# Performance work log

Measured on AMD Instinct MI355X. Metric: run time of the kernel, lower is better.

The kernel has to match this reference:

```python
import jax, jax.numpy as jnp
import numpy as np

HOPS = 3
VOCAB, EMBD, STORY_LEN, SENT_LEN, BATCH, QLEN = 50000, 128, 200, 32, 64, 32
INIT_RNG = 0.1


def setup_inputs() -> dict:
    key = jax.random.key(0)
    k1, k2, k3, k4, k5 = jax.random.split(key, 5)
    x = jax.random.randint(k1, (BATCH, STORY_LEN, SENT_LEN), 0, VOCAB)          # story token ids
    q = jax.random.randint(k2, (BATCH, QLEN), 0, VOCAB)                          # question token ids
    # hops+1 embedding tables, initialized ~ Normal(mean=-0.1, std=0.1) as in the torch code
    A = jax.random.normal(k3, (HOPS + 1, VOCAB, EMBD), dtype=jnp.float32) * INIT_RNG - INIT_RNG
    TA = jax.random.normal(k4, (STORY_LEN,), dtype=jnp.float32) * INIT_RNG - INIT_RNG
    TC = jax.random.normal(k5, (STORY_LEN,), dtype=jnp.float32) * INIT_RNG - INIT_RNG
    return {"A": A, "TA": TA, "TC": TC, "x": x, "q": q}


def reference(A, TA, TC, x, q):
    # dropout p=0.0 -> identity
    # u: question embedding, summed over query tokens -> [B, E]
    u = jnp.take(A[1], q, axis=0).sum(axis=1)
    for k in range(HOPS):
        # memory (m) and output (c) representations: gather + sum over sentence tokens + temporal encoding
        m = jnp.take(A[k], x, axis=0).sum(axis=2) + TA[None, :, None]      # [B, S, E]
        c = jnp.take(A[k + 1], x, axis=0).sum(axis=2) + TC[None, :, None]  # [B, S, E]
        p = jax.nn.softmax(jnp.einsum("bse,be->bs", m, u), axis=-1)        # attention over story [B, S]
        u = jnp.einsum("bse,bs->be", c, p) + u                              # weighted combine + residual
    logits = u @ A[HOPS].T                                                  # W = A[-1].weight.T -> [B, V]
    return jax.nn.log_softmax(logits, axis=-1)
```

## Files before the change

kernel.cpp:

```cpp
#include <hip/hip_runtime.h>
#include <math.h>

#define VOCAB 50000
#define EMBD  128
#define SLEN  200
#define TOK   32
#define BATCH 64
#define QLEN  32
#define NSENT (BATCH*SLEN)
#define NTASK (4*NSENT + BATCH)
#define TBL   ((size_t)VOCAB*EMBD)
#define VT    32
#define NTILE ((VOCAB + VT - 1)/VT)

__device__ inline float bits2f(unsigned u){ union{unsigned u; float f;}c; c.u=u; return c.f; }
__device__ inline unsigned f2bits(float f){ union{float f; unsigned u;}c; c.f=f; return c.u; }
__device__ inline unsigned pack_bf16(float lo, float hi){
    unsigned ul = f2bits(lo), uh = f2bits(hi);
    unsigned rl = (ul + 0x7fffu + ((ul>>16)&1u)) >> 16;
    unsigned rh = (uh + 0x7fffu + ((uh>>16)&1u)) >> 16;
    return rl | (rh<<16);
}

__device__ inline float waveSum(float v) {
    #pragma unroll
    for (int o = 32; o > 0; o >>= 1) v += __shfl_down(v, o, 64);
    return v;
}
__device__ inline float waveMax(float v) {
    #pragma unroll
    for (int o = 32; o > 0; o >>= 1) v = fmaxf(v, __shfl_down(v, o, 64));
    return v;
}

__global__ __launch_bounds__(256) void conv_kernel(
    const float* __restrict__ A, unsigned* __restrict__ Ab)
{
    size_t i = ((size_t)blockIdx.x*256 + threadIdx.x)*8;
    float4 a = *(const float4*)(A+i);
    float4 b = *(const float4*)(A+i+4);
    uint4 o;
    o.x = pack_bf16(a.x,a.y); o.y = pack_bf16(a.z,a.w);
    o.z = pack_bf16(b.x,b.y); o.w = pack_bf16(b.z,b.w);
    *(uint4*)(Ab + i/2) = o;
}

__global__ __launch_bounds__(256) void gather_kernel(
    const unsigned* __restrict__ Ab, const int* __restrict__ x,
    const int* __restrict__ q, float* __restrict__ G, float* __restrict__ uF)
{
    int w    = blockIdx.x * 4 + (threadIdx.x >> 6);
    int lane = threadIdx.x & 63;
    const int*      idxp;
    const unsigned* tbl;
    float*          outp;
    if (w < 4 * NSENT) {
        int k  = w / NSENT;
        int bs = w - k * NSENT;
        idxp = x + (size_t)bs * TOK;
        tbl  = Ab + (size_t)k * (TBL/2);
        outp = G + (size_t)w * EMBD;
    } else {
        int b = w - 4 * NSENT;
        idxp = q + (size_t)b * QLEN;
        tbl  = Ab + (TBL/2);
        outp = uF + (size_t)b * EMBD;
    }
    int tg = lane >> 4;
    int sl = lane & 15;
    int idxs[8];
    #pragma unroll
    for (int i = 0; i < 8; i++) idxs[i] = idxp[i*4 + tg];
    float acc[8];
    #pragma unroll
    for (int c = 0; c < 8; c++) acc[c] = 0.f;
    #pragma unroll
    for (int i = 0; i < 8; i++) {
        uint4 v = *(const uint4*)(tbl + (size_t)idxs[i]*64 + sl*4);
        acc[0] += bits2f(v.x<<16); acc[1] += bits2f(v.x&0xffff0000u);
        acc[2] += bits2f(v.y<<16); acc[3] += bits2f(v.y&0xffff0000u);
        acc[4] += bits2f(v.z<<16); acc[5] += bits2f(v.z&0xffff0000u);
        acc[6] += bits2f(v.w<<16); acc[7] += bits2f(v.w&0xffff0000u);
    }
    #pragma unroll
    for (int c = 0; c < 8; c++) {
        acc[c] += __shfl_xor(acc[c], 32, 64);
        acc[c] += __shfl_xor(acc[c], 16, 64);
    }
    if (lane < 32) {
        int g = lane & 15, h = lane >> 4;
        float4 r; r.x = acc[4*h]; r.y = acc[4*h+1]; r.z = acc[4*h+2]; r.w = acc[4*h+3];
        ((float4*)outp)[2*g + h] = r;
    }
}

__global__ __launch_bounds__(1024) void hops_kernel(
    const float* __restrict__ G, float* __restrict__ u,
    const float* __restrict__ TA, const float* __restrict__ TC)
{
    int b = blockIdx.x;
    int t = threadIdx.x;
    int lane = t & 63, wid = t >> 6;
    __shared__ __align__(16) float uL[EMBD];
    __shared__ float p[256];
    __shared__ float red[16], red2[16];
    __shared__ float pc[7*EMBD];

    if (t < EMBD) uL[t] = u[(size_t)b * EMBD + t];
    __syncthreads();

    for (int k = 0; k < 3; k++) {
        float v = (t < EMBD) ? uL[t] : 0.f;
        v = waveSum(v);
        if (lane == 0) red[wid] = v;
        __syncthreads();
        float sumU = 0.f;
        #pragma unroll
        for (int i = 0; i < 16; i++) sumU += red[i];
        int s = t >> 2, qd = t & 3;
        if (s < SLEN) {
            const float4* g4 = (const float4*)(G + ((size_t)k*NSENT + (size_t)b*SLEN + s)*EMBD);
            const float4* u4 = (const float4*)uL;
            float dot = 0.f;
            #pragma unroll
            for (int e = 0; e < 8; e++) {
                float4 gg = g4[qd*8+e], uu = u4[qd*8+e];
                dot += gg.x*uu.x + gg.y*uu.y + gg.z*uu.z + gg.w*uu.w;
            }
            dot += __shfl_xor(dot, 1, 64);
            dot += __shfl_xor(dot, 2, 64);
            if (qd == 0) p[s] = dot + TA[s]*sumU;
        }
        __syncthreads();
        float mv = (t < SLEN) ? p[t] : -3.4e38f;
        mv = waveMax(mv);
        if (lane == 0) red[wid] = mv;
        __syncthreads();
        float M = -3.4e38f;
        #pragma unroll
        for (int i = 0; i < 16; i++) M = fmaxf(M, red[i]);
        __syncthreads();
        float ev = 0.f, tc = 0.f;
        if (t < SLEN) { ev = __expf(p[t] - M); p[t] = ev; tc = ev * TC[t]; }
        float sv = waveSum(ev);
        float tv = waveSum(tc);
        if (lane == 0) { red[wid] = sv; red2[wid] = tv; }
        __syncthreads();
        float sumP = 0.f, pTC = 0.f;
        #pragma unroll
        for (int i = 0; i < 16; i++) { sumP += red[i]; pTC += red2[i]; }
        const float* Gc = G + ((size_t)(k+1)*NSENT + (size_t)b*SLEN)*EMBD;
        int e = t & 127, ch = t >> 7;
        float acc = 0.f;
        for (int s2 = ch*25; s2 < ch*25 + 25; s2++)
            acc += p[s2] * Gc[(size_t)s2*EMBD + e];
        if (ch > 0) pc[(ch-1)*EMBD + e] = acc;
        __syncthreads();
        if (ch == 0) {
            #pragma unroll
            for (int c = 0; c < 7; c++) acc += pc[c*EMBD + e];
            uL[e] += (acc + pTC) / sumP;
        }
        __syncthreads();
    }
    if (t < EMBD) u[(size_t)b * EMBD + t] = uL[t];
}

__global__ __launch_bounds__(256) void logits_kernel(
    const unsigned* __restrict__ A3b, const float* __restrict__ u,
    float* __restrict__ out, float* __restrict__ part)
{
    __shared__ __align__(16) float Us[BATCH * EMBD];
    __shared__ __align__(16) float As[VT * 132];
    int t  = threadIdx.x;
    int v0 = blockIdx.x * VT;
    #pragma unroll
    for (int pp = 0; pp < 8; pp++) {
        int f = t * 4 + pp * 1024;
        *(float4*)&Us[f] = *(const float4*)&u[f];
    }
    {
        int f = t * 16;
        int r = f >> 7, c = f & 127;
        int vv = v0 + r;
        float vals[16];
        if (vv < VOCAB) {
            const unsigned* src = A3b + (size_t)vv*64 + (c>>1);
            uint4 p0 = *(const uint4*)src;
            uint4 p1 = *(const uint4*)(src + 4);
            vals[0]=bits2f(p0.x<<16);  vals[1]=bits2f(p0.x&0xffff0000u);
            vals[2]=bits2f(p0.y<<16);  vals[3]=bits2f(p0.y&0xffff0000u);
            vals[4]=bits2f(p0.z<<16);  vals[5]=bits2f(p0.z&0xffff0000u);
            vals[6]=bits2f(p0.w<<16);  vals[7]=bits2f(p0.w&0xffff0000u);
            vals[8]=bits2f(p1.x<<16);  vals[9]=bits2f(p1.x&0xffff0000u);
            vals[10]=bits2f(p1.y<<16); vals[11]=bits2f(p1.y&0xffff0000u);
            vals[12]=bits2f(p1.z<<16); vals[13]=bits2f(p1.z&0xffff0000u);
            vals[14]=bits2f(p1.w<<16); vals[15]=bits2f(p1.w&0xffff0000u);
        } else {
            #pragma unroll
            for (int i = 0; i < 16; i++) vals[i] = 0.f;
        }
        #pragma unroll
        for (int i = 0; i < 16; i += 4)
            *(float4*)&As[r*132 + c + i] = *(float4*)&vals[i];
    }
    __syncthreads();
    int lane = t & 63, w = t >> 6;
    int tx = lane & 15, ty = lane >> 4;
    int bb = w * 16 + ty * 4;
    float acc[4][2];
    #pragma unroll
    for (int i = 0; i < 4; i++) { acc[i][0] = 0.f; acc[i][1] = 0.f; }
    for (int k = 0; k < EMBD; k += 4) {
        float4 a[2], uu[4];
        a[0] = *(float4*)&As[tx * 132 + k];
        a[1] = *(float4*)&As[(tx + 16) * 132 + k];
        #pragma unroll
        for (int i = 0; i < 4; i++) uu[i] = *(float4*)&Us[(bb + i) * EMBD + k];
        #pragma unroll
        for (int i = 0; i < 4; i++)
            #pragma unroll
            for (int j = 0; j < 2; j++)
                acc[i][j] += uu[i].x * a[j].x + uu[i].y * a[j].y
                           + uu[i].z * a[j].z + uu[i].w * a[j].w;
    }
    bool val0 = (v0 + tx) < VOCAB, val1 = (v0 + tx + 16) < VOCAB;
    #pragma unroll
    for (int i = 0; i < 4; i++) {
        int bI = bb + i;
        if (val0) out[(size_t)bI * VOCAB + v0 + tx]      = acc[i][0];
        if (val1) out[(size_t)bI * VOCAB + v0 + tx + 16] = acc[i][1];
        float m = fmaxf(val0 ? acc[i][0] : -3.4e38f, val1 ? acc[i][1] : -3.4e38f);
        #pragma unroll
        for (int o = 1; o < 16; o <<= 1) m = fmaxf(m, __shfl_xor(m, o, 64));
        float se = (val0 ? __expf(acc[i][0] - m) : 0.f)
                 + (val1 ? __expf(acc[i][1] - m) : 0.f);
        #pragma unroll
        for (int o = 1; o < 16; o <<= 1) se += __shfl_xor(se, o, 64);
        if (tx == 0) {
            float2 pr; pr.x = m; pr.y = se;
            ((float2*)part)[(size_t)bI * NTILE + blockIdx.x] = pr;
        }
    }
}

__global__ __launch_bounds__(256) void lse_kernel(
    const float* __restrict__ part, float* __restrict__ lse)
{
    int r = blockIdx.x, t = threadIdx.x;
    int lane = t & 63, wid = t >> 6;
    __shared__ float sm[4], sl[4];
    const float2* P = (const float2*)part + (size_t)r * NTILE;
    float M = -3.4e38f, L = 0.f;
    for (int i = t; i < NTILE; i += 256) {
        float2 pr = P[i];
        float m2 = fmaxf(M, pr.x);
        L = L * __expf(M - m2) + pr.y * __expf(pr.x - m2);
        M = m2;
    }
    #pragma unroll
    for (int o = 1; o < 64; o <<= 1) {
        float Mo = __shfl_xor(M, o, 64), Lo = __shfl_xor(L, o, 64);
        float m2 = fmaxf(M, Mo);
        L = L * __expf(M - m2) + Lo * __expf(Mo - m2);
        M = m2;
    }
    if (lane == 0) { sm[wid] = M; sl[wid] = L; }
    __syncthreads();
    if (t == 0) {
        float Mf = -3.4e38f, Lf = 0.f;
        #pragma unroll
        for (int i = 0; i < 4; i++) {
            float m2 = fmaxf(Mf, sm[i]);
            Lf = Lf * __expf(Mf - m2) + sl[i] * __expf(sm[i] - m2);
            Mf = m2;
        }
        lse[r] = Mf + __logf(Lf);
    }
}

__global__ __launch_bounds__(256) void norm_kernel(
    float* __restrict__ out, const float* __restrict__ lse)
{
    int gid = blockIdx.x * 256 + threadIdx.x;
    int b = gid / (VOCAB/4);
    float l = lse[b];
    float4 v = ((float4*)out)[gid];
    v.x -= l; v.y -= l; v.z -= l; v.w -= l;
    ((float4*)out)[gid] = v;
}

extern "C" void kernel_launch(void* const* d_in, const int* in_sizes, int n_in,
                              void* d_out, int out_size, void* d_ws, size_t ws_size,
                              hipStream_t stream)
{
    const float* A  = (const float*)d_in[0];
    const float* TA = (const float*)d_in[1];
    const float* TC = (const float*)d_in[2];
    const int*   x  = (const int*)d_in[3];
    const int*   q  = (const int*)d_in[4];
    float* out = (float*)d_out;

    unsigned* Ab = (unsigned*)d_ws;
    float* G   = (float*)((char*)d_ws + (size_t)4*TBL*2);
    float* uF  = G + (size_t)4*NSENT*EMBD;
    float* part= uF + (size_t)BATCH*EMBD;
    float* lse = part + (size_t)BATCH*NTILE*2;

    conv_kernel  <<<12500, 256, 0, stream>>>(A, Ab);
    gather_kernel<<<NTASK/4, 256, 0, stream>>>(Ab, x, q, G, uF);
    hops_kernel  <<<BATCH, 1024, 0, stream>>>(G, uF, TA, TC);
    logits_kernel<<<NTILE, 256, 0, stream>>>(Ab + 3*(TBL/2), uF, out, part);
    lse_kernel   <<<BATCH, 256, 0, stream>>>(part, lse);
    norm_kernel  <<<BATCH*(VOCAB/4)/256, 256, 0, stream>>>(out, lse);
}
```

Before: 283.4 us.

## Use bf16 MFMA for logits, cache G in LDS across hops, fuse lse into norm

```diff
diff --git a/kernel.cpp b/kernel.cpp
--- a/kernel.cpp
+++ b/kernel.cpp
@@ -10,8 +10,10 @@
 #define NSENT (BATCH*SLEN)
 #define NTASK (4*NSENT + BATCH)
 #define TBL   ((size_t)VOCAB*EMBD)
-#define VT    32
-#define NTILE ((VOCAB + VT - 1)/VT)
+#define NTILE 3125
+
+typedef short short8 __attribute__((ext_vector_type(8)));
+typedef float f32x4  __attribute__((ext_vector_type(4)));
 
 __device__ inline float bits2f(unsigned u){ union{unsigned u; float f;}c; c.u=u; return c.f; }
 __device__ inline unsigned f2bits(float f){ union{float f; unsigned u;}c; c.f=f; return c.u; }
@@ -21,6 +23,10 @@
     unsigned rh = (uh + 0x7fffu + ((uh>>16)&1u)) >> 16;
     return rl | (rh<<16);
 }
+__device__ inline unsigned short bf16of(float f){
+    unsigned u = f2bits(f);
+    return (unsigned short)((u + 0x7fffu + ((u>>16)&1u)) >> 16);
+}
 
 __device__ inline float waveSum(float v) {
     #pragma unroll
@@ -49,12 +55,22 @@
     const unsigned* __restrict__ Ab, const int* __restrict__ x,
     const int* __restrict__ q, float* __restrict__ G, float* __restrict__ uF)
 {
-    int w    = blockIdx.x * 4 + (threadIdx.x >> 6);
+    int B = blockIdx.x;
+    int wid = threadIdx.x >> 6;
+    int w;
+    if (B < 12800) {
+        int k = (B & 7) >> 1;
+        int i = (B >> 3)*2 + (B & 1);
+        w = k*NSENT + i*4 + wid;
+    } else {
+        w = B*4 + wid;
+    }
     int lane = threadIdx.x & 63;
     const int*      idxp;
     const unsigned* tbl;
-    float*          outp;
-    if (w < 4 * NSENT) {
+    bool qtask = (w >= 4*NSENT);
+    float* outp;
+    if (!qtask) {
         int k  = w / NSENT;
         int bs = w - k * NSENT;
         idxp = x + (size_t)bs * TOK;
@@ -95,18 +111,20 @@
 }
 
 __global__ __launch_bounds__(1024) void hops_kernel(
-    const float* __restrict__ G, float* __restrict__ u,
-    const float* __restrict__ TA, const float* __restrict__ TC)
+    const float* __restrict__ G, const float* __restrict__ uF,
+    const float* __restrict__ TA, const float* __restrict__ TC,
+    unsigned short* __restrict__ ub)
 {
     int b = blockIdx.x;
     int t = threadIdx.x;
     int lane = t & 63, wid = t >> 6;
+    __shared__ __align__(16) float Gs[SLEN*132];
     __shared__ __align__(16) float uL[EMBD];
     __shared__ float p[256];
     __shared__ float red[16], red2[16];
     __shared__ float pc[7*EMBD];
 
-    if (t < EMBD) uL[t] = u[(size_t)b * EMBD + t];
+    if (t < EMBD) uL[t] = uF[(size_t)b * EMBD + t];
     __syncthreads();
 
     for (int k = 0; k < 3; k++) {
@@ -119,13 +137,22 @@
         for (int i = 0; i < 16; i++) sumU += red[i];
         int s = t >> 2, qd = t & 3;
         if (s < SLEN) {
-            const float4* g4 = (const float4*)(G + ((size_t)k*NSENT + (size_t)b*SLEN + s)*EMBD);
             const float4* u4 = (const float4*)uL;
             float dot = 0.f;
-            #pragma unroll
-            for (int e = 0; e < 8; e++) {
-                float4 gg = g4[qd*8+e], uu = u4[qd*8+e];
-                dot += gg.x*uu.x + gg.y*uu.y + gg.z*uu.z + gg.w*uu.w;
+            if (k == 0) {
+                const float4* g4 = (const float4*)(G + ((size_t)b*SLEN + s)*EMBD);
+                #pragma unroll
+                for (int e = 0; e < 8; e++) {
+                    float4 gg = g4[qd*8+e], uu = u4[qd*8+e];
+                    dot += gg.x*uu.x + gg.y*uu.y + gg.z*uu.z + gg.w*uu.w;
+                }
+            } else {
+                const float4* g4 = (const float4*)(Gs + s*132);
+                #pragma unroll
+                for (int e = 0; e < 8; e++) {
+                    float4 gg = g4[qd*8+e], uu = u4[qd*8+e];
+                    dot += gg.x*uu.x + gg.y*uu.y + gg.z*uu.z + gg.w*uu.w;
+                }
             }
             dot += __shfl_xor(dot, 1, 64);
             dot += __shfl_xor(dot, 2, 64);
@@ -152,8 +179,11 @@
         const float* Gc = G + ((size_t)(k+1)*NSENT + (size_t)b*SLEN)*EMBD;
         int e = t & 127, ch = t >> 7;
         float acc = 0.f;
-        for (int s2 = ch*25; s2 < ch*25 + 25; s2++)
-            acc += p[s2] * Gc[(size_t)s2*EMBD + e];
+        for (int s2 = ch*25; s2 < ch*25 + 25; s2++) {
+            float g = Gc[(size_t)s2*EMBD + e];
+            Gs[s2*132 + e] = g;
+            acc += p[s2] * g;
+        }
         if (ch > 0) pc[(ch-1)*EMBD + e] = acc;
         __syncthreads();
         if (ch == 0) {
@@ -163,94 +193,69 @@
         }
         __syncthreads();
     }
-    if (t < EMBD) u[(size_t)b * EMBD + t] = uL[t];
-}
-
-__global__ __launch_bounds__(256) void logits_kernel(
-    const unsigned* __restrict__ A3b, const float* __restrict__ u,
+    if (t < EMBD) ub[(size_t)b * EMBD + t] = bf16of(uL[t]);
+}
+
+__global__ __launch_bounds__(256) void logits_mfma(
+    const unsigned short* __restrict__ A3b, const unsigned short* __restrict__ ub,
     float* __restrict__ out, float* __restrict__ part)
 {
-    __shared__ __align__(16) float Us[BATCH * EMBD];
-    __shared__ __align__(16) float As[VT * 132];
-    int t  = threadIdx.x;
-    int v0 = blockIdx.x * VT;
-    #pragma unroll
-    for (int pp = 0; pp < 8; pp++) {
-        int f = t * 4 + pp * 1024;
-        *(float4*)&Us[f] = *(const float4*)&u[f];
-    }
-    {
-        int f = t * 16;
-        int r = f >> 7, c = f & 127;
-        int vv = v0 + r;
-        float vals[16];
-        if (vv < VOCAB) {
-            const unsigned* src = A3b + (size_t)vv*64 + (c>>1);
-            uint4 p0 = *(const uint4*)src;
-            uint4 p1 = *(const uint4*)(src + 4);
-            vals[0]=bits2f(p0.x<<16);  vals[1]=bits2f(p0.x&0xffff0000u);
-            vals[2]=bits2f(p0.y<<16);  vals[3]=bits2f(p0.y&0xffff0000u);
-            vals[4]=bits2f(p0.z<<16);  vals[5]=bits2f(p0.z&0xffff0000u);
-            vals[6]=bits2f(p0.w<<16);  vals[7]=bits2f(p0.w&0xffff0000u);
-            vals[8]=bits2f(p1.x<<16);  vals[9]=bits2f(p1.x&0xffff0000u);
-            vals[10]=bits2f(p1.y<<16); vals[11]=bits2f(p1.y&0xffff0000u);
-            vals[12]=bits2f(p1.z<<16); vals[13]=bits2f(p1.z&0xffff0000u);
-            vals[14]=bits2f(p1.w<<16); vals[15]=bits2f(p1.w&0xffff0000u);
-        } else {
+    int w = blockIdx.x*4 + (threadIdx.x >> 6);
+    if (w >= NTILE) return;
+    int lane = threadIdx.x & 63;
+    int col = lane & 15, quad = lane >> 4;
+    int v0 = w * 16;
+
+    short8 af[4][4];
+    #pragma unroll
+    for (int bt = 0; bt < 4; bt++)
+        #pragma unroll
+        for (int kc = 0; kc < 4; kc++)
+            af[bt][kc] = *(const short8*)(ub + (bt*16 + col)*EMBD + kc*32 + quad*8);
+
+    f32x4 acc[4];
+    #pragma unroll
+    for (int bt = 0; bt < 4; bt++) acc[bt] = (f32x4){0.f, 0.f, 0.f, 0.f};
+
+    #pragma unroll
+    for (int kc = 0; kc < 4; kc++) {
+        short8 bf = *(const short8*)(A3b + (size_t)(v0 + col)*EMBD + kc*32 + quad*8);
+        #pragma unroll
+        for (int bt = 0; bt < 4; bt++)
+            acc[bt] = __builtin_amdgcn_mfma_f32_16x16x32_bf16(af[bt][kc], bf, acc[bt], 0, 0, 0);
+    }
+
+    #pragma unroll
+    for (int bt = 0; bt < 4; bt++) {
+        #pragma unroll
+        for (int r = 0; r < 4; r++) {
+            int bI = bt*16 + quad*4 + r;
+            out[(size_t)bI * VOCAB + v0 + col] = acc[bt][r];
+        }
+        #pragma unroll
+        for (int r = 0; r < 4; r++) {
+            float m = acc[bt][r];
             #pragma unroll
-            for (int i = 0; i < 16; i++) vals[i] = 0.f;
-        }
-        #pragma unroll
-        for (int i = 0; i < 16; i += 4)
-            *(float4*)&As[r*132 + c + i] = *(float4*)&vals[i];
-    }
-    __syncthreads();
-    int lane = t & 63, w = t >> 6;
-    int tx = lane & 15, ty = lane >> 4;
-    int bb = w * 16 + ty * 4;
-    float acc[4][2];
-    #pragma unroll
-    for (int i = 0; i < 4; i++) { acc[i][0] = 0.f; acc[i][1] = 0.f; }
-    for (int k = 0; k < EMBD; k += 4) {
-        float4 a[2], uu[4];
-        a[0] = *(float4*)&As[tx * 132 + k];
-        a[1] = *(float4*)&As[(tx + 16) * 132 + k];
-        #pragma unroll
-        for (int i = 0; i < 4; i++) uu[i] = *(float4*)&Us[(bb + i) * EMBD + k];
-        #pragma unroll
-        for (int i = 0; i < 4; i++)
+            for (int o = 1; o < 16; o <<= 1) m = fmaxf(m, __shfl_xor(m, o, 64));
+            float se = __expf(acc[bt][r] - m);
             #pragma unroll
-            for (int j = 0; j < 2; j++)
-                acc[i][j] += uu[i].x * a[j].x + uu[i].y * a[j].y
-                           + uu[i].z * a[j].z + uu[i].w * a[j].w;
-    }
-    bool val0 = (v0 + tx) < VOCAB, val1 = (v0 + tx + 16) < VOCAB;
-    #pragma unroll
-    for (int i = 0; i < 4; i++) {
-        int bI = bb + i;
-        if (val0) out[(size_t)bI * VOCAB + v0 + tx]      = acc[i][0];
-        if (val1) out[(size_t)bI * VOCAB + v0 + tx + 16] = acc[i][1];
-        float m = fmaxf(val0 ? acc[i][0] : -3.4e38f, val1 ? acc[i][1] : -3.4e38f);
-        #pragma unroll
-        for (int o = 1; o < 16; o <<= 1) m = fmaxf(m, __shfl_xor(m, o, 64));
-        float se = (val0 ? __expf(acc[i][0] - m) : 0.f)
-                 + (val1 ? __expf(acc[i][1] - m) : 0.f);
-        #pragma unroll
-        for (int o = 1; o < 16; o <<= 1) se += __shfl_xor(se, o, 64);
-        if (tx == 0) {
-            float2 pr; pr.x = m; pr.y = se;
-            ((float2*)part)[(size_t)bI * NTILE + blockIdx.x] = pr;
-        }
-    }
-}
-
-__global__ __launch_bounds__(256) void lse_kernel(
-    const float* __restrict__ part, float* __restrict__ lse)
-{
-    int r = blockIdx.x, t = threadIdx.x;
-    int lane = t & 63, wid = t >> 6;
+            for (int o = 1; o < 16; o <<= 1) se += __shfl_xor(se, o, 64);
+            if (col == 0) {
+                int bI = bt*16 + quad*4 + r;
+                float2 pr; pr.x = m; pr.y = se;
+                ((float2*)part)[(size_t)bI * NTILE + w] = pr;
+            }
+        }
+    }
+}
+
+__global__ __launch_bounds__(256) void norm_kernel(
+    float* __restrict__ out, const float* __restrict__ part)
+{
+    int b = blockIdx.x / 49, c = blockIdx.x % 49;
+    int t = threadIdx.x, lane = t & 63, wid = t >> 6;
     __shared__ float sm[4], sl[4];
-    const float2* P = (const float2*)part + (size_t)r * NTILE;
+    const float2* P = (const float2*)part + (size_t)b * NTILE;
     float M = -3.4e38f, L = 0.f;
     for (int i = t; i < NTILE; i += 256) {
         float2 pr = P[i];
@@ -267,27 +272,21 @@
     }
     if (lane == 0) { sm[wid] = M; sl[wid] = L; }
     __syncthreads();
-    if (t == 0) {
-        float Mf = -3.4e38f, Lf = 0.f;
-        #pragma unroll
-        for (int i = 0; i < 4; i++) {
-            float m2 = fmaxf(Mf, sm[i]);
-            Lf = Lf * __expf(Mf - m2) + sl[i] * __expf(sm[i] - m2);
-            Mf = m2;
-        }
-        lse[r] = Mf + __logf(Lf);
-    }
-}
-
-__global__ __launch_bounds__(256) void norm_kernel(
-    float* __restrict__ out, const float* __restrict__ lse)
-{
-    int gid = blockIdx.x * 256 + threadIdx.x;
-    int b = gid / (VOCAB/4);
-    float l = lse[b];
-    float4 v = ((float4*)out)[gid];
-    v.x -= l; v.y -= l; v.z -= l; v.w -= l;
-    ((float4*)out)[gid] = v;
+    float Mf = -3.4e38f, Lf = 0.f;
+    #pragma unroll
+    for (int i = 0; i < 4; i++) {
+        float m2 = fmaxf(Mf, sm[i]);
+        Lf = Lf * __expf(Mf - m2) + sl[i] * __expf(sm[i] - m2);
+        Mf = m2;
+    }
+    float lse = Mf + __logf(Lf);
+    int f4 = c * 256 + t;
+    if (f4 < VOCAB/4) {
+        float4* rowp = (float4*)(out + (size_t)b * VOCAB);
+        float4 v = rowp[f4];
+        v.x -= lse; v.y -= lse; v.z -= lse; v.w -= lse;
+        rowp[f4] = v;
+    }
 }
 
 extern "C" void kernel_launch(void* const* d_in, const int* in_sizes, int n_in,
@@ -304,13 +303,13 @@
     unsigned* Ab = (unsigned*)d_ws;
     float* G   = (float*)((char*)d_ws + (size_t)4*TBL*2);
     float* uF  = G + (size_t)4*NSENT*EMBD;
-    float* part= uF + (size_t)BATCH*EMBD;
-    float* lse = part + (size_t)BATCH*NTILE*2;
+    unsigned short* ubp = (unsigned short*)(uF + (size_t)BATCH*EMBD);
+    float* part = (float*)(ubp + (size_t)BATCH*EMBD);
 
     conv_kernel  <<<12500, 256, 0, stream>>>(A, Ab);
     gather_kernel<<<NTASK/4, 256, 0, stream>>>(Ab, x, q, G, uF);
-    hops_kernel  <<<BATCH, 1024, 0, stream>>>(G, uF, TA, TC);
-    logits_kernel<<<NTILE, 256, 0, stream>>>(Ab + 3*(TBL/2), uF, out, part);
-    lse_kernel   <<<BATCH, 256, 0, stream>>>(part, lse);
-    norm_kernel  <<<BATCH*(VOCAB/4)/256, 256, 0, stream>>>(out, lse);
-}
+    hops_kernel  <<<BATCH, 1024, 0, stream>>>(G, uF, TA, TC, ubp);
+    logits_mfma  <<<(NTILE+3)/4, 256, 0, stream>>>(
+        (const unsigned short*)Ab + (size_t)3*TBL, ubp, out, part);
+    norm_kernel  <<<BATCH*49, 256, 0, stream>>>(out, part);
+}
```

Result: faster. 277.7 us (-2.0%).
